# Performance work log

Hardware: AMD Instinct MI355X
Metric: run time of the kernel (lower is better)

Reference implementation:

```python
import jax, jax.numpy as jnp
import numpy as np

B, T, DIN, H = 32, 4096, 256, 256


def _log_g(x):
    # log of g(x) = where(x>=0, x+0.5, sigmoid(x)), computed stably in log space
    return jnp.where(x >= 0.0, jnp.log(jax.nn.relu(x) + 0.5), -jax.nn.softplus(-x))


def setup_inputs() -> dict:
    key = jax.random.key(0)
    ks = jax.random.split(key, 4)
    scale = (6.0 / (DIN + H)) ** 0.5  # xavier_uniform
    return {
        "x": jax.random.normal(ks[0], (B, T, DIN), dtype=jnp.float32),
        "h0": jax.random.normal(ks[1], (B, 1, H), dtype=jnp.float32),
        "Wz": jax.random.uniform(ks[2], (H, DIN), jnp.float32, -scale, scale),
        "bz": jnp.zeros((H,), jnp.float32),
        "Wh": jax.random.uniform(ks[3], (H, DIN), jnp.float32, -scale, scale),
        "bh": jnp.zeros((H,), jnp.float32),
    }


def reference(x, h0, Wz, bz, Wh, bh):
    # minGRU training path: log-space parallel scan (Heinsen scan)
    k = jnp.einsum("bti,hi->bth", x, Wz) + bz            # pre-activation of z gate
    log_z = -jax.nn.softplus(-k)                           # log sigmoid(k)
    log_coeffs = -jax.nn.softplus(k)                       # log(1 - sigmoid(k))
    log_h0 = _log_g(h0)                                    # (B,1,H)
    log_tilde_h = _log_g(jnp.einsum("bti,hi->bth", x, Wh) + bh)
    log_values = jnp.concatenate([log_h0, log_z + log_tilde_h], axis=1)  # (B,T+1,H)
    # a_star[t] = sum_{s<=t} log_coeffs[s], with a leading zero
    a_star = jnp.cumsum(jnp.pad(log_coeffs, ((0, 0), (1, 0), (0, 0))), axis=1)
    # logcumsumexp along time via associative scan with logaddexp
    lcse = jax.lax.associative_scan(jnp.logaddexp, log_values - a_star, axis=1)
    log_h = a_star + lcse                                  # (B,T+1,H)
    return jnp.exp(log_h[:, 1:])                           # (B,T,H)
```

## Files before the change

### kernel.cpp

```cpp
#include <hip/hip_runtime.h>
#include <hip/hip_fp16.h>

typedef __attribute__((ext_vector_type(8))) short short8;
typedef __attribute__((ext_vector_type(4))) float f32x4;
typedef unsigned short ushort_t;
typedef unsigned int uint_t;

#define B_SZ 32
#define T_SZ 4096
#define D_IN 256
#define H_SZ 256
#define M_SZ (B_SZ * T_SZ)
#define CHUNK 64
#define NCHUNK (T_SZ / CHUNK)

__device__ __forceinline__ ushort_t f2bf(float f) {
  unsigned int u = __float_as_uint(f);
  unsigned int r = (u + 0x7FFFu + ((u >> 16) & 1u)) >> 16;
  return (ushort_t)r;
}

__device__ __forceinline__ float sigmoidf_(float xv) {
  float e = __expf(-fabsf(xv));
  float s = 1.0f / (1.0f + e);
  return xv >= 0.0f ? s : 1.0f - s;
}

__device__ __forceinline__ float unpack_lo(uint_t pk) {
  return __half2float(__ushort_as_half((ushort_t)(pk & 0xFFFFu)));
}
__device__ __forceinline__ float unpack_hi(uint_t pk) {
  return __half2float(__ushort_as_half((ushort_t)(pk >> 16)));
}

__global__ void prep_w(const float* __restrict__ Wz, const float* __restrict__ Wh,
                       ushort_t* __restrict__ wsB) {
  int g = blockIdx.x * 256 + threadIdx.x;
  if (g >= 8 * 2048) return;
  int ks = g >> 11;
  int r = g & 2047;
  int c = r >> 9;
  int n = r & 511;
  int h = (n >> 5) * 16 + (n & 15);
  const float* W = ((n >> 4) & 1) ? Wh : Wz;
  const float* src = W + (size_t)h * D_IN + ks * 32 + c * 8;
  ushort_t* dst = wsB + (size_t)g * 8;
#pragma unroll
  for (int j = 0; j < 8; ++j) dst[j] = f2bf(src[j]);
}

__global__ __launch_bounds__(512, 4) void gemm_av(
    const float* __restrict__ x, const ushort_t* __restrict__ wsB,
    const float* __restrict__ bz, const float* __restrict__ bh,
    uint_t* __restrict__ av, float2* cAV) {
  __shared__ __align__(16) unsigned char lds[73728];
  ushort_t* As = (ushort_t*)lds;
  ushort_t* Bs = (ushort_t*)(lds + 8192);

  const int tid = threadIdx.x;
  const int lane = tid & 63;
  const int wid = tid >> 6;
  const int m0 = blockIdx.x * 64;

  const int a_row = tid & 63;
  const int a_g = tid >> 6;
  const float* asrc = x + (size_t)(m0 + a_row) * D_IN + a_g * 8;

  f32x4 acc[4][4];
#pragma unroll
  for (int rt = 0; rt < 4; ++rt)
#pragma unroll
    for (int ct = 0; ct < 4; ++ct) {
      f32x4 z4 = {0.f, 0.f, 0.f, 0.f};
      acc[rt][ct] = z4;
    }

  {
    const ushort_t* bsrc = wsB + (size_t)wid * 2048 + lane * 8;
    ushort_t* bdst = Bs + wid * 2048;
#pragma unroll
    for (int cc = 0; cc < 4; ++cc) {
      __builtin_amdgcn_global_load_lds(
          (const __attribute__((address_space(1))) void*)(bsrc + cc * 512),
          (__attribute__((address_space(3))) void*)(bdst + cc * 512), 16, 0, 0);
    }
    if (tid < 256) {
      float4 f0 = *(const float4*)(asrc);
      float4 f1 = *(const float4*)(asrc + 4);
      union { ushort_t e[8]; short8 s; } cv;
      cv.e[0] = f2bf(f0.x); cv.e[1] = f2bf(f0.y);
      cv.e[2] = f2bf(f0.z); cv.e[3] = f2bf(f0.w);
      cv.e[4] = f2bf(f1.x); cv.e[5] = f2bf(f1.y);
      cv.e[6] = f2bf(f1.z); cv.e[7] = f2bf(f1.w);
      *(short8*)(As + tid * 8) = cv.s;
    }
  }
  __syncthreads();

#pragma unroll
  for (int ks = 0; ks < 8; ++ks) {
    const int cur = ks & 1;
    short8 afr[4], bfr[4];
    {
      const int c = lane >> 4;
      const int r16 = lane & 15;
#pragma unroll
      for (int rt = 0; rt < 4; ++rt) {
        int row = rt * 16 + r16;
        afr[rt] = *(const short8*)(As + cur * 2048 + (c * 64 + row) * 8);
      }
#pragma unroll
      for (int ct = 0; ct < 4; ++ct) {
        int n = wid * 64 + ct * 16 + r16;
        bfr[ct] = *(const short8*)(Bs + cur * 16384 + (c * 512 + n) * 8);
      }
    }
    float4 nf0, nf1;
    if (ks < 7) {
      const ushort_t* bsrc = wsB + (size_t)(ks + 1) * 16384 + wid * 2048 + lane * 8;
      ushort_t* bdst = Bs + (cur ^ 1) * 16384 + wid * 2048;
#pragma unroll
      for (int cc = 0; cc < 4; ++cc) {
        __builtin_amdgcn_global_load_lds(
            (const __attribute__((address_space(1))) void*)(bsrc + cc * 512),
            (__attribute__((address_space(3))) void*)(bdst + cc * 512), 16, 0, 0);
      }
      if (tid < 256) {
        nf0 = *(const float4*)(asrc + (ks + 1) * 32);
        nf1 = *(const float4*)(asrc + (ks + 1) * 32 + 4);
      }
    }
#pragma unroll
    for (int rt = 0; rt < 4; ++rt)
#pragma unroll
      for (int ct = 0; ct < 4; ++ct)
        acc[rt][ct] = __builtin_amdgcn_mfma_f32_16x16x32_bf16(
            afr[rt], bfr[ct], acc[rt][ct], 0, 0, 0);
    if (ks < 7 && tid < 256) {
      union { ushort_t e[8]; short8 s; } cv;
      cv.e[0] = f2bf(nf0.x); cv.e[1] = f2bf(nf0.y);
      cv.e[2] = f2bf(nf0.z); cv.e[3] = f2bf(nf0.w);
      cv.e[4] = f2bf(nf1.x); cv.e[5] = f2bf(nf1.y);
      cv.e[6] = f2bf(nf1.z); cv.e[7] = f2bf(nf1.w);
      *(short8*)(As + (cur ^ 1) * 2048 + tid * 8) = cv.s;
    }
    __syncthreads();
  }

  const int col16 = lane & 15;
  const int rgrp = lane >> 4;
#pragma unroll
  for (int i = 0; i < 2; ++i) {
    int hh = (wid * 2 + i) * 16 + col16;
    float bzv = bz[hh];
    float bhv = bh[hh];
    float CA = 1.0f, CV = 0.0f;
#pragma unroll
    for (int rt = 0; rt < 4; ++rt) {
      float A4 = 1.0f, V4 = 0.0f;
#pragma unroll
      for (int j = 0; j < 4; ++j) {
        int row = m0 + rt * 16 + rgrp * 4 + j;
        float kv = acc[rt][2 * i][j] + bzv;
        float pv = acc[rt][2 * i + 1][j] + bhv;
        float a = sigmoidf_(-kv);
        float z = 1.0f - a;
        float gg = (pv >= 0.0f) ? (pv + 0.5f) : sigmoidf_(pv);
        float vv = z * gg;
        uint_t pk = (uint_t)__half_as_ushort(__float2half_rn(a)) |
                    ((uint_t)__half_as_ushort(__float2half_rn(vv)) << 16);
        av[(size_t)row * H_SZ + hh] = pk;
        V4 = fmaf(a, V4, vv);
        A4 *= a;
      }
      float Ap = __shfl_xor(A4, 16);
      float Vp = __shfl_xor(V4, 16);
      float A8 = A4 * Ap;
      float V8 = (lane & 16) ? fmaf(A4, Vp, V4) : fmaf(Ap, V4, Vp);
      float Ap2 = __shfl_xor(A8, 32);
      float Vp2 = __shfl_xor(V8, 32);
      float A16 = A8 * Ap2;
      float V16 = (lane & 32) ? fmaf(A8, Vp2, V8) : fmaf(Ap2, V8, Vp2);
      CV = fmaf(A16, CV, V16);
      CA = CA * A16;
    }
    if (cAV != nullptr && lane < 16) {
      float2 r; r.x = CA; r.y = CV;
      cAV[(size_t)blockIdx.x * H_SZ + hh] = r;
    }
  }
}

__global__ __launch_bounds__(256) void chunk_carry(
    const float* __restrict__ h0, const float2* __restrict__ cAV,
    float* __restrict__ hb) {
  const int b = blockIdx.x;
  const int h = threadIdx.x;
  float v0 = h0[b * H_SZ + h];
  float hc = (v0 >= 0.0f) ? (v0 + 0.5f) : sigmoidf_(v0);

  const float2* p = cAV + (size_t)b * NCHUNK * H_SZ + h;
  float* o = hb + (size_t)b * NCHUNK * H_SZ + h;

  float2 buf[NCHUNK];
#pragma unroll
  for (int c = 0; c < NCHUNK; ++c) buf[c] = p[(size_t)c * H_SZ];

#pragma unroll
  for (int c = 0; c < NCHUNK; ++c) {
    o[(size_t)c * H_SZ] = hc;
    hc = fmaf(buf[c].x, hc, buf[c].y);
  }
}

__global__ __launch_bounds__(256) void chunk_scan_out(
    const uint_t* av, const float* __restrict__ hb, float* out) {
  const int b = blockIdx.x >> 6;
  const int c = blockIdx.x & 63;
  const int h = threadIdx.x;

  float hc = hb[((size_t)b * NCHUNK + c) * H_SZ + h];
  const uint_t* p = av + ((size_t)b * T_SZ + c * CHUNK) * H_SZ + h;
  float* o = out + ((size_t)b * T_SZ + c * CHUNK) * H_SZ + h;

  uint_t buf[CHUNK];
#pragma unroll
  for (int s = 0; s < CHUNK; ++s) buf[s] = p[(size_t)s * H_SZ];

#pragma unroll
  for (int s = 0; s < CHUNK; ++s) {
    float a = unpack_lo(buf[s]);
    float v = unpack_hi(buf[s]);
    hc = fmaf(a, hc, v);
    o[(size_t)s * H_SZ] = hc;
  }
}

__global__ __launch_bounds__(64) void scan_seq(const float* __restrict__ h0,
                                               const uint_t* av, float* out) {
  const int b = blockIdx.x >> 2;
  const int hg = blockIdx.x & 3;
  const int h = hg * 64 + threadIdx.x;

  float v0 = h0[b * H_SZ + h];
  float hc = (v0 >= 0.0f) ? (v0 + 0.5f) : sigmoidf_(v0);

  const uint_t* p = av + (size_t)b * T_SZ * H_SZ + h;
  float* o = out + (size_t)b * T_SZ * H_SZ + h;

  uint_t buf[32];
#pragma unroll
  for (int d = 0; d < 32; ++d) buf[d] = p[(size_t)d * H_SZ];

  for (int t0 = 0; t0 < T_SZ; t0 += 32) {
#pragma unroll
    for (int d = 0; d < 32; ++d) {
      int t = t0 + d;
      uint_t pk = buf[d];
      int tn = t + 32;
      if (tn < T_SZ) buf[d] = p[(size_t)tn * H_SZ];
      hc = fmaf(unpack_lo(pk), hc, unpack_hi(pk));
      o[(size_t)t * H_SZ] = hc;
    }
  }
}

extern "C" void kernel_launch(void* const* d_in, const int* in_sizes, int n_in,
                              void* d_out, int out_size, void* d_ws, size_t ws_size,
                              hipStream_t stream) {
  const float* x  = (const float*)d_in[0];
  const float* h0 = (const float*)d_in[1];
  const float* Wz = (const float*)d_in[2];
  const float* bz = (const float*)d_in[3];
  const float* Wh = (const float*)d_in[4];
  const float* bh = (const float*)d_in[5];
  float* out = (float*)d_out;

  const size_t wsBBytes = 262144;
  const size_t cavBytes = (size_t)B_SZ * NCHUNK * H_SZ * 8;
  const size_t hbBytes  = (size_t)B_SZ * NCHUNK * H_SZ * 4;
  const size_t avOff    = 8388608;
  const size_t avBytes  = (size_t)M_SZ * H_SZ * 4;

  ushort_t* wsB = (ushort_t*)d_ws;
  float2* cAV = (float2*)((char*)d_ws + wsBBytes);
  float* hb   = (float*)((char*)d_ws + wsBBytes + cavBytes);

  const bool haveSummaries = ws_size >= wsBBytes + cavBytes + hbBytes;
  uint_t* av;
  if (ws_size >= avOff + avBytes) {
    av = (uint_t*)((char*)d_ws + avOff);
  } else {
    av = (uint_t*)d_out;
  }

  prep_w<<<64, 256, 0, stream>>>(Wz, Wh, wsB);
  gemm_av<<<M_SZ / 64, 512, 0, stream>>>(x, wsB, bz, bh, av,
                                         haveSummaries ? cAV : (float2*)nullptr);
  if (haveSummaries) {
    chunk_carry<<<B_SZ, 256, 0, stream>>>(h0, cAV, hb);
    chunk_scan_out<<<B_SZ * NCHUNK, 256, 0, stream>>>(av, hb, out);
  } else {
    scan_seq<<<B_SZ * 4, 64, 0, stream>>>(h0, av, out);
  }
}
```

Measured before the change: 163.4 us.

## Prefetch all x K-slices into registers upfront and spread A conversion across all threads

The GEMM kernel now issues every float4 load of its x tile at kernel start into eight registers per thread, instead of loading one K-slice per iteration. All 512 threads now take part, each converting half of an 8-element group, where previously only 256 did. This is meant to hide global load latency behind the whole MFMA loop and to balance the conversion work across threads. The cost is roughly 32 extra VGPRs per thread, which could hurt occupancy under launch_bounds(512,4).

New measurement: 166.0 us. Within noise of the previous version (+1.6%).

```diff
diff --git a/kernel.cpp b/kernel.cpp
--- a/kernel.cpp
+++ b/kernel.cpp
@@ -62,9 +62,14 @@
   const int wid = tid >> 6;
   const int m0 = blockIdx.x * 64;
 
-  const int a_row = tid & 63;
-  const int a_g = tid >> 6;
-  const float* asrc = x + (size_t)(m0 + a_row) * D_IN + a_g * 8;
+  const int a_row = (tid >> 1) & 63;
+  const int a_c = tid >> 7;
+  const int a_half = tid & 1;
+  const float* asrc = x + (size_t)(m0 + a_row) * D_IN + a_c * 8 + a_half * 4;
+
+  float4 pf[8];
+#pragma unroll
+  for (int ks = 0; ks < 8; ++ks) pf[ks] = *(const float4*)(asrc + ks * 32);
 
   f32x4 acc[4][4];
 #pragma unroll
@@ -84,16 +89,10 @@
           (const __attribute__((address_space(1))) void*)(bsrc + cc * 512),
           (__attribute__((address_space(3))) void*)(bdst + cc * 512), 16, 0, 0);
     }
-    if (tid < 256) {
-      float4 f0 = *(const float4*)(asrc);
-      float4 f1 = *(const float4*)(asrc + 4);
-      union { ushort_t e[8]; short8 s; } cv;
-      cv.e[0] = f2bf(f0.x); cv.e[1] = f2bf(f0.y);
-      cv.e[2] = f2bf(f0.z); cv.e[3] = f2bf(f0.w);
-      cv.e[4] = f2bf(f1.x); cv.e[5] = f2bf(f1.y);
-      cv.e[6] = f2bf(f1.z); cv.e[7] = f2bf(f1.w);
-      *(short8*)(As + tid * 8) = cv.s;
-    }
+    uint2 w;
+    w.x = (uint_t)f2bf(pf[0].x) | ((uint_t)f2bf(pf[0].y) << 16);
+    w.y = (uint_t)f2bf(pf[0].z) | ((uint_t)f2bf(pf[0].w) << 16);
+    *(uint2*)((char*)As + tid * 8) = w;
   }
   __syncthreads();
 
@@ -115,7 +114,6 @@
         bfr[ct] = *(const short8*)(Bs + cur * 16384 + (c * 512 + n) * 8);
       }
     }
-    float4 nf0, nf1;
     if (ks < 7) {
       const ushort_t* bsrc = wsB + (size_t)(ks + 1) * 16384 + wid * 2048 + lane * 8;
       ushort_t* bdst = Bs + (cur ^ 1) * 16384 + wid * 2048;
@@ -125,10 +123,6 @@
             (const __attribute__((address_space(1))) void*)(bsrc + cc * 512),
             (__attribute__((address_space(3))) void*)(bdst + cc * 512), 16, 0, 0);
       }
-      if (tid < 256) {
-        nf0 = *(const float4*)(asrc + (ks + 1) * 32);
-        nf1 = *(const float4*)(asrc + (ks + 1) * 32 + 4);
-      }
     }
 #pragma unroll
     for (int rt = 0; rt < 4; ++rt)
@@ -136,13 +130,11 @@
       for (int ct = 0; ct < 4; ++ct)
         acc[rt][ct] = __builtin_amdgcn_mfma_f32_16x16x32_bf16(
             afr[rt], bfr[ct], acc[rt][ct], 0, 0, 0);
-    if (ks < 7 && tid < 256) {
-      union { ushort_t e[8]; short8 s; } cv;
-      cv.e[0] = f2bf(nf0.x); cv.e[1] = f2bf(nf0.y);
-      cv.e[2] = f2bf(nf0.z); cv.e[3] = f2bf(nf0.w);
-      cv.e[4] = f2bf(nf1.x); cv.e[5] = f2bf(nf1.y);
-      cv.e[6] = f2bf(nf1.z); cv.e[7] = f2bf(nf1.w);
-      *(short8*)(As + (cur ^ 1) * 2048 + tid * 8) = cv.s;
+    if (ks < 7) {
+      uint2 w;
+      w.x = (uint_t)f2bf(pf[ks + 1].x) | ((uint_t)f2bf(pf[ks + 1].y) << 16);
+      w.y = (uint_t)f2bf(pf[ks + 1].z) | ((uint_t)f2bf(pf[ks + 1].w) << 16);
+      *(uint2*)((char*)As + (cur ^ 1) * 4096 + tid * 8) = w;
     }
     __syncthreads();
   }
```

## Split GEMM N dimension across two blocks of 256 threads each

Applied to the files above, without the earlier changes.

Each 64-row M tile of the gate GEMM is now split across two blocks that each compute half of the 512 interleaved z/h columns, using 4 waves instead of 8. The LDS footprint drops from 72KB to 40KB per block and the grid doubles, which raises occupancy and block-level parallelism. In exchange, each x row tile is loaded from global memory and converted to bf16 twice, once per block.

New measurement: 182.9 us. 1.12x slower.

```diff
diff --git a/kernel.cpp b/kernel.cpp
--- a/kernel.cpp
+++ b/kernel.cpp
@@ -49,51 +49,55 @@
   for (int j = 0; j < 8; ++j) dst[j] = f2bf(src[j]);
 }
 
-__global__ __launch_bounds__(512, 4) void gemm_av(
+__global__ __launch_bounds__(256, 4) void gemm_av(
     const float* __restrict__ x, const ushort_t* __restrict__ wsB,
     const float* __restrict__ bz, const float* __restrict__ bh,
     uint_t* __restrict__ av, float2* cAV) {
-  __shared__ __align__(16) unsigned char lds[73728];
+  __shared__ __align__(16) unsigned char lds[40960];
   ushort_t* As = (ushort_t*)lds;
   ushort_t* Bs = (ushort_t*)(lds + 8192);
 
   const int tid = threadIdx.x;
   const int lane = tid & 63;
   const int wid = tid >> 6;
-  const int m0 = blockIdx.x * 64;
+  const int bid = blockIdx.x;
+  const int m0 = (bid >> 1) * 64;
+  const int n0 = (bid & 1) * 256;
 
   const int a_row = tid & 63;
-  const int a_g = tid >> 6;
-  const float* asrc = x + (size_t)(m0 + a_row) * D_IN + a_g * 8;
-
-  f32x4 acc[4][4];
-#pragma unroll
-  for (int rt = 0; rt < 4; ++rt)
-#pragma unroll
-    for (int ct = 0; ct < 4; ++ct) {
-      f32x4 z4 = {0.f, 0.f, 0.f, 0.f};
-      acc[rt][ct] = z4;
-    }
-
-  {
-    const ushort_t* bsrc = wsB + (size_t)wid * 2048 + lane * 8;
-    ushort_t* bdst = Bs + wid * 2048;
+  const int a_c = tid >> 6;
+  const float* asrc = x + (size_t)(m0 + a_row) * D_IN + a_c * 8;
+
+  auto STAGE_B = [&](int ks, int buf) {
+    const ushort_t* bsrc = wsB + ((size_t)ks * 2048 + wid * 512 + n0) * 8 + lane * 8;
+    ushort_t* bdst = Bs + buf * 8192 + (wid * 256) * 8;
 #pragma unroll
     for (int cc = 0; cc < 4; ++cc) {
       __builtin_amdgcn_global_load_lds(
           (const __attribute__((address_space(1))) void*)(bsrc + cc * 512),
           (__attribute__((address_space(3))) void*)(bdst + cc * 512), 16, 0, 0);
     }
-    if (tid < 256) {
-      float4 f0 = *(const float4*)(asrc);
-      float4 f1 = *(const float4*)(asrc + 4);
-      union { ushort_t e[8]; short8 s; } cv;
-      cv.e[0] = f2bf(f0.x); cv.e[1] = f2bf(f0.y);
-      cv.e[2] = f2bf(f0.z); cv.e[3] = f2bf(f0.w);
-      cv.e[4] = f2bf(f1.x); cv.e[5] = f2bf(f1.y);
-      cv.e[6] = f2bf(f1.z); cv.e[7] = f2bf(f1.w);
-      *(short8*)(As + tid * 8) = cv.s;
-    }
+  };
+
+  f32x4 acc[4][4];
+#pragma unroll
+  for (int rt = 0; rt < 4; ++rt)
+#pragma unroll
+    for (int ct = 0; ct < 4; ++ct) {
+      f32x4 z4 = {0.f, 0.f, 0.f, 0.f};
+      acc[rt][ct] = z4;
+    }
+
+  STAGE_B(0, 0);
+  {
+    float4 f0 = *(const float4*)(asrc);
+    float4 f1 = *(const float4*)(asrc + 4);
+    union { ushort_t e[8]; short8 s; } cv;
+    cv.e[0] = f2bf(f0.x); cv.e[1] = f2bf(f0.y);
+    cv.e[2] = f2bf(f0.z); cv.e[3] = f2bf(f0.w);
+    cv.e[4] = f2bf(f1.x); cv.e[5] = f2bf(f1.y);
+    cv.e[6] = f2bf(f1.z); cv.e[7] = f2bf(f1.w);
+    *(short8*)(As + tid * 8) = cv.s;
   }
   __syncthreads();
 
@@ -111,24 +115,15 @@
       }
 #pragma unroll
       for (int ct = 0; ct < 4; ++ct) {
-        int n = wid * 64 + ct * 16 + r16;
-        bfr[ct] = *(const short8*)(Bs + cur * 16384 + (c * 512 + n) * 8);
+        int nn = wid * 64 + ct * 16 + r16;
+        bfr[ct] = *(const short8*)(Bs + cur * 8192 + (c * 256 + nn) * 8);
       }
     }
     float4 nf0, nf1;
     if (ks < 7) {
-      const ushort_t* bsrc = wsB + (size_t)(ks + 1) * 16384 + wid * 2048 + lane * 8;
-      ushort_t* bdst = Bs + (cur ^ 1) * 16384 + wid * 2048;
-#pragma unroll
-      for (int cc = 0; cc < 4; ++cc) {
-        __builtin_amdgcn_global_load_lds(
-            (const __attribute__((address_space(1))) void*)(bsrc + cc * 512),
-            (__attribute__((address_space(3))) void*)(bdst + cc * 512), 16, 0, 0);
-      }
-      if (tid < 256) {
-        nf0 = *(const float4*)(asrc + (ks + 1) * 32);
-        nf1 = *(const float4*)(asrc + (ks + 1) * 32 + 4);
-      }
+      STAGE_B(ks + 1, cur ^ 1);
+      nf0 = *(const float4*)(asrc + (ks + 1) * 32);
+      nf1 = *(const float4*)(asrc + (ks + 1) * 32 + 4);
     }
 #pragma unroll
     for (int rt = 0; rt < 4; ++rt)
@@ -136,7 +131,7 @@
       for (int ct = 0; ct < 4; ++ct)
         acc[rt][ct] = __builtin_amdgcn_mfma_f32_16x16x32_bf16(
             afr[rt], bfr[ct], acc[rt][ct], 0, 0, 0);
-    if (ks < 7 && tid < 256) {
+    if (ks < 7) {
       union { ushort_t e[8]; short8 s; } cv;
       cv.e[0] = f2bf(nf0.x); cv.e[1] = f2bf(nf0.y);
       cv.e[2] = f2bf(nf0.z); cv.e[3] = f2bf(nf0.w);
@@ -151,7 +146,7 @@
   const int rgrp = lane >> 4;
 #pragma unroll
   for (int i = 0; i < 2; ++i) {
-    int hh = (wid * 2 + i) * 16 + col16;
+    int hh = (bid & 1) * 128 + (wid * 2 + i) * 16 + col16;
     float bzv = bz[hh];
     float bhv = bh[hh];
     float CA = 1.0f, CV = 0.0f;
@@ -186,7 +181,7 @@
     }
     if (cAV != nullptr && lane < 16) {
       float2 r; r.x = CA; r.y = CV;
-      cAV[(size_t)blockIdx.x * H_SZ + hh] = r;
+      cAV[(size_t)(bid >> 1) * H_SZ + hh] = r;
     }
   }
 }
@@ -295,8 +290,8 @@
   }
 
   prep_w<<<64, 256, 0, stream>>>(Wz, Wh, wsB);
-  gemm_av<<<M_SZ / 64, 512, 0, stream>>>(x, wsB, bz, bh, av,
-                                         haveSummaries ? cAV : (float2*)nullptr);
+  gemm_av<<<(M_SZ / 64) * 2, 256, 0, stream>>>(x, wsB, bz, bh, av,
+                                               haveSummaries ? cAV : (float2*)nullptr);
   if (haveSummaries) {
     chunk_carry<<<B_SZ, 256, 0, stream>>>(h0, cAV, hb);
     chunk_scan_out<<<B_SZ * NCHUNK, 256, 0, stream>>>(av, hb, out);
```
